# Kernel tuning notes

Measured on AMD Instinct MI355X. Metric: run time of the kernel, lower is better.

Reference implementation:

```python
import jax, jax.numpy as jnp
import numpy as np

N_ELEC, N_NUC, D, F, E = 1024, 256, 64, 64, 131072
HH, HG = 128, 128
# labels: en (elec->nuc), ne (nuc->elec), same (elec->elec), anti (elec->elec)
SRC_N = [N_ELEC, N_NUC, N_ELEC, N_ELEC]
TGT_N = [N_NUC, N_ELEC, N_ELEC, N_ELEC]


def setup_inputs() -> dict:
    key = jax.random.key(0)
    ks = jax.random.split(key, 16)
    s_elec = jax.random.normal(ks[0], (N_ELEC, D), jnp.float32)
    v_elec = jax.random.normal(ks[1], (N_ELEC, D, 3), jnp.float32)
    s_nuc = jax.random.normal(ks[2], (N_NUC, D), jnp.float32)
    v_nuc = jax.random.normal(ks[3], (N_NUC, D, 3), jnp.float32)
    senders = jnp.stack([jax.random.randint(jax.random.fold_in(ks[4], i), (E,), 0, SRC_N[i]) for i in range(4)]).astype(jnp.int32)
    receivers = jnp.stack([jax.random.randint(jax.random.fold_in(ks[5], i), (E,), 0, TGT_N[i]) for i in range(4)]).astype(jnp.int32)
    dist = jax.random.uniform(ks[6], (4, E, F), jnp.float32)
    dirs = jax.random.normal(ks[7], (4, E, 3), jnp.float32)
    dirs = dirs / jnp.linalg.norm(dirs, axis=-1, keepdims=True)  # unit directions
    def w_init(k, shape):
        return jax.random.normal(k, shape, jnp.float32) / jnp.sqrt(jnp.float32(shape[-2]))
    return {
        's_elec': s_elec, 'v_elec': v_elec, 's_nuc': s_nuc, 'v_nuc': v_nuc,
        'dist': dist, 'dirs': dirs,
        'W_w': w_init(ks[8], (4, F, 3 * D)),
        'W_h1': w_init(ks[9], (4, D, HH)), 'W_h2': w_init(ks[10], (4, HH, 3 * D)),
        'W_g1': w_init(ks[11], (4, 2 * D, HG)), 'W_g2': w_init(ks[12], (4, HG, 3 * D)),
        'W_V': jnp.broadcast_to(jnp.eye(D, dtype=jnp.float32), (4, D, D)),
        'W_U': jnp.broadcast_to(jnp.eye(D, dtype=jnp.float32), (4, D, D)),
        'senders': senders, 'receivers': receivers,
    }


def _painn_layer(s_elec, v_elec, s_nuc, v_nuc, dist, dirs, W_w, W_h1, W_h2, W_g1, W_g2, W_V, W_U, senders, receivers):
    src_s = [s_elec, s_nuc, s_elec, s_elec]
    src_v = [v_elec, v_nuc, v_elec, v_elec]
    ds_e = jnp.zeros_like(s_elec); dv_e = jnp.zeros_like(v_elec)
    ds_n = jnp.zeros_like(s_nuc); dv_n = jnp.zeros_like(v_nuc)
    for i in range(4):
        n_tgt = TGT_N[i]
        # edge MLPs: w (1-layer, last linear) and h (2-layer silu, last linear), bias-free
        we = dist[i] @ W_w[i]                                   # [E, 3D]
        h_all = jax.nn.silu(src_s[i] @ W_h1[i]) @ W_h2[i]        # [n_src, 3D]
        hx = h_all[senders[i]]                                   # gather per edge
        phi_s, phi_vv, phi_vs = jnp.split(we * hx, 3, axis=-1)   # each [E, D]
        z_s = jax.ops.segment_sum(phi_s, receivers[i], n_tgt)    # [n_tgt, D]
        vv = phi_vv[..., None] * src_v[i][senders[i]]            # [E, D, 3]
        vs = phi_vs[..., None] * dirs[i][:, None, :]             # [E, D, 3]
        z_v = jax.ops.segment_sum(vv + vs, receivers[i], n_tgt)  # [n_tgt, D, 3]
        Vv = jnp.einsum('ndi,df->nfi', z_v, W_V[i])
        Uv = jnp.einsum('ndi,df->nfi', z_v, W_U[i])
        g_in = jnp.concatenate([z_s, (Vv ** 2).sum(axis=-1)], axis=-1)  # [n_tgt, 2D]
        gs = jax.nn.silu(g_in @ W_g1[i]) @ W_g2[i]               # [n_tgt, 3D]
        a_ss, a_vv, a_sv = jnp.split(gs, 3, axis=-1)
        upd_v = Uv * a_vv[..., None]
        upd_s = a_sv * jnp.einsum('nfi,nfi->nf', Uv, Vv) + a_ss
        if i == 0:  # 'en' -> nuclei
            ds_n = ds_n + upd_s; dv_n = dv_n + upd_v
        else:       # 'ne','same','anti' -> electrons
            ds_e = ds_e + upd_s; dv_e = dv_e + upd_v
    s_e = s_elec + ds_e
    v_e = v_elec + dv_e
    return jnp.concatenate([s_e, v_e.reshape(N_ELEC, -1)], axis=-1)


def reference(s_elec, v_elec, s_nuc, v_nuc, dist, dirs, W_w, W_h1, W_h2, W_g1, W_g2, W_V, W_U, senders, receivers):
    return _painn_layer(s_elec, v_elec, s_nuc, v_nuc, dist, dirs, W_w, W_h1, W_h2, W_g1, W_g2, W_V, W_U, senders, receivers)
```

## Files before the change

### kernel.cpp

```cpp
#include <hip/hip_runtime.h>
#include <stdint.h>

#define E_EDGES 131072
#define NELEC 1024
#define NNUC 256
#define MAXCHUNK 256
#define ECHUNK 128
#define NBLK 16
#define UNPB 4

typedef unsigned short ushort_t;
typedef __attribute__((ext_vector_type(8))) short short8;
typedef __attribute__((ext_vector_type(4))) short short4_t;
typedef __attribute__((ext_vector_type(4))) float float4_t;
typedef __attribute__((ext_vector_type(8))) float float8_t;
typedef __attribute__((ext_vector_type(4))) int int4_t;
typedef __attribute__((ext_vector_type(2))) unsigned int uint2_t;

__device__ inline float silu_f(float x){ return x / (1.0f + expf(-x)); }

__device__ inline short f2bf_rne(float x){
    union { float f; uint32_t u; } a; a.f = x;
    return (short)((a.u + 0x7fffu + ((a.u >> 16) & 1u)) >> 16);
}
__device__ inline float bf2f(short h){
    union { uint32_t u; float f; } a; a.u = ((uint32_t)(uint16_t)h) << 16;
    return a.f;
}
__device__ inline ushort_t bfu(float x){ return (ushort_t)f2bf_rne(x); }
__device__ inline float asf_lo(uint32_t u){ union { uint32_t u; float f; } a; a.u = u << 16; return a.f; }
__device__ inline float asf_hi(uint32_t u){ union { uint32_t u; float f; } a; a.u = u & 0xFFFF0000u; return a.f; }

__global__ __launch_bounds__(256) void prep_kernel(
    const float* __restrict__ s_elec, const float* __restrict__ v_elec,
    const float* __restrict__ s_nuc,  const float* __restrict__ v_nuc,
    const float* __restrict__ W_h1, const float* __restrict__ W_h2,
    const float* __restrict__ W_w,
    const int* __restrict__ receivers,
    ushort_t* __restrict__ tabA, ushort_t* __restrict__ tabB,
    short* __restrict__ fragH, short* __restrict__ fragL,
    int* __restrict__ bh, float* __restrict__ out)
{
    int b = blockIdx.x, tid = threadIdx.x;
    __shared__ float sls[8][64];
    __shared__ float hidls[128][8];
    __shared__ int hist[1024];

    if (b < 288){
        int t, node0;
        if (b < 32){ t = 0; node0 = b*8; }
        else if (b < 160){ t = 1; node0 = (b-32)*8; }
        else { t = 2; node0 = (b-160)*8; }
        int tp = t + 1;
        const float* src = (t == 0) ? s_nuc : s_elec;
        const float* vsrc = (t == 0) ? v_nuc : v_elec;
        long baseA = (t == 0) ? 0 : (t == 1 ? 32768 : 163840);
        long baseB = (t == 0) ? 0 : (t == 1 ? 65536 : 327680);
        for (int i = tid; i < 512; i += 256){ int n = i >> 6, f = i & 63; sls[n][f] = src[(node0+n)*64 + f]; }
        __syncthreads();
        {
            int j = tid & 127, nh = tid >> 7;
            const float* w1 = W_h1 + (long)tp*64*128;
            float a0=0,a1=0,a2=0,a3=0;
            #pragma unroll 8
            for (int f = 0; f < 64; f++){
                float w = w1[f*128 + j];
                a0 += sls[nh*4+0][f]*w; a1 += sls[nh*4+1][f]*w;
                a2 += sls[nh*4+2][f]*w; a3 += sls[nh*4+3][f]*w;
            }
            float4_t hv = { silu_f(a0), silu_f(a1), silu_f(a2), silu_f(a3) };
            *(float4_t*)&hidls[j][nh*4] = hv;
        }
        __syncthreads();
        if (tid < 192){
            const float* w2 = W_h2 + (long)tp*128*192;
            float acc[8] = {0,0,0,0,0,0,0,0};
            #pragma unroll 4
            for (int h = 0; h < 128; h++){
                float w = w2[h*192 + tid];
                float4_t ha = *(float4_t*)&hidls[h][0];
                float4_t hb = *(float4_t*)&hidls[h][4];
                acc[0]+=ha[0]*w; acc[1]+=ha[1]*w; acc[2]+=ha[2]*w; acc[3]+=ha[3]*w;
                acc[4]+=hb[0]*w; acc[5]+=hb[1]*w; acc[6]+=hb[2]*w; acc[7]+=hb[3]*w;
            }
            int p = tid >> 6, d2 = tid & 63;
            if (p == 0){
                #pragma unroll
                for (int n = 0; n < 8; n++)
                    tabA[baseA + (long)((node0+n)*64 + d2)*2 + 0] = bfu(acc[n]);
            } else if (p == 2){
                #pragma unroll
                for (int n = 0; n < 8; n++)
                    tabA[baseA + (long)((node0+n)*64 + d2)*2 + 1] = bfu(acc[n]);
            } else {
                #pragma unroll
                for (int n = 0; n < 8; n++){
                    const float* vp = vsrc + (long)(node0+n)*192 + d2*3;
                    long o = baseB + (long)((node0+n)*64 + d2)*4;
                    tabB[o+0] = bfu(acc[n]*vp[0]);
                    tabB[o+1] = bfu(acc[n]*vp[1]);
                    tabB[o+2] = bfu(acc[n]*vp[2]);
                }
            }
        }
    } else if (b < 291){
        int t = b - 288, tp = t + 1;
        const float* W = W_w + (long)tp*64*192;
        for (int idx = tid; idx < 12288; idx += 256){
            int j    = idx & 7;
            int lane = (idx >> 3) & 63;
            int ks   = (idx >> 9) & 1;
            int nt   = idx >> 10;
            int k = ks*32 + ((lane >> 4) & 3)*8 + j;
            int n = nt*16 + (lane & 15);
            float v = W[k*192 + n];
            short hi = f2bf_rne(v);
            short lo = f2bf_rne(v - bf2f(hi));
            fragH[t*12288 + idx] = hi;
            fragL[t*12288 + idx] = lo;
        }
    } else if (b < 547){
        int i = (b - 291)*256 + tid;
        int n = i >> 6, c4 = i & 63;
        float4_t v;
        if (c4 < 16) v = *(const float4_t*)(s_elec + n*64 + c4*4);
        else         v = *(const float4_t*)(v_elec + n*192 + (c4-16)*4);
        *(float4_t*)(out + n*256 + c4*4) = v;
    } else {
        int hb = b - 547, t = hb >> 4, blk = hb & 15;
        for (int i = tid; i < 1024; i += 256) hist[i] = 0;
        __syncthreads();
        long base = (long)(t+1)*E_EDGES + blk*8192;
        #pragma unroll 4
        for (int it = 0; it < 32; it++){
            int r = receivers[base + it*256 + tid];
            atomicAdd(&hist[r], 1);
        }
        __syncthreads();
        for (int bin = tid; bin < 1024; bin += 256)
            bh[(t*1024 + bin)*NBLK + blk] = hist[bin];
    }
}

__global__ __launch_bounds__(1024) void scan_kernel(int* __restrict__ bh,
                                                    int* __restrict__ offs,
                                                    int* __restrict__ counts){
    __shared__ int buf[1024];
    int t = blockIdx.x;
    int tid = threadIdx.x;
    int base = (t*1024 + tid)*NBLK;
    int vals[NBLK];
    const int4_t* p = (const int4_t*)(bh + base);
    int s = 0;
    #pragma unroll
    for (int j = 0; j < NBLK/4; j++){
        int4_t x = p[j];
        vals[j*4+0]=x[0]; vals[j*4+1]=x[1]; vals[j*4+2]=x[2]; vals[j*4+3]=x[3];
        s += x[0]+x[1]+x[2]+x[3];
    }
    buf[tid] = s;
    __syncthreads();
    int x = s;
    for (int off = 1; off < 1024; off <<= 1){
        int y = (tid >= off) ? buf[tid - off] : 0;
        __syncthreads();
        x += y; buf[tid] = x;
        __syncthreads();
    }
    int run = t*E_EDGES + (x - s);
    offs[t*1024 + tid] = run;
    counts[t*1024 + tid] = s;
    #pragma unroll
    for (int j = 0; j < NBLK; j++){
        bh[base + j] = run;
        run += vals[j];
    }
}

__global__ __launch_bounds__(256) void scatter_kernel(const int* __restrict__ receivers,
                                                      const int* __restrict__ senders,
                                                      const int* __restrict__ bh,
                                                      int* __restrict__ sorted){
    int hb = blockIdx.x, t = hb >> 4, blk = hb & 15;
    int tid = threadIdx.x;
    __shared__ int cur[1024];
    for (int bin = tid; bin < 1024; bin += 256) cur[bin] = bh[(t*1024 + bin)*NBLK + blk];
    __syncthreads();
    long base = (long)(t+1)*E_EDGES + blk*8192;
    #pragma unroll 2
    for (int it = 0; it < 32; it++){
        int e = blk*8192 + it*256 + tid;
        int r = receivers[base + it*256 + tid];
        int snd = senders[base + it*256 + tid];
        int pos = atomicAdd(&cur[r], 1);
        sorted[pos] = e | (snd << 17);
    }
}

__global__ __launch_bounds__(256) void edge_kernel(
    const float* __restrict__ dist, const float* __restrict__ dirs,
    const ushort_t* __restrict__ tabA, const ushort_t* __restrict__ tabB,
    const short* __restrict__ fragH, const short* __restrict__ fragL,
    const int* __restrict__ counts, const int* __restrict__ offs, const int* __restrict__ sorted,
    float* __restrict__ zbuf)
{
    int b = blockIdx.x;
    int t = b >> 10, node = b & 1023;
    const ushort_t* ta = tabA + ((t == 0) ? 0 : (t == 1 ? 32768 : 163840));
    const ushort_t* tb = tabB + ((t == 0) ? 0 : (t == 1 ? 65536 : 327680));
    const float* dbase = dist + (long)(t+1)*E_EDGES*64;
    const float* dirbase = dirs + (long)(t+1)*E_EDGES*3;

    int tid = threadIdx.x;
    int w = tid >> 6, l = tid & 63;
    int q = l >> 4, c16 = l & 15;
    int d = w*16 + c16;
    int se = tid >> 1, sk = tid & 1;

    __shared__ short AHs[ECHUNK*64];
    __shared__ short ALs[ECHUNK*64];
    __shared__ int sid[ECHUNK];
    __shared__ float dls[ECHUNK][3];

    short8 bhf[3][2], blf[3][2];
    #pragma unroll
    for (int ni = 0; ni < 3; ni++){
        int nt = w + ni*4;
        #pragma unroll
        for (int ks = 0; ks < 2; ks++){
            long base = (long)t*12288 + ((nt*2 + ks)*64 + l)*8;
            bhf[ni][ks] = *(const short8*)(fragH + base);
            blf[ni][ks] = *(const short8*)(fragL + base);
        }
    }

    float acc_s = 0.f, acc_v0 = 0.f, acc_v1 = 0.f, acc_v2 = 0.f;

    int deg   = counts[t*1024 + node];
    int start = offs[t*1024 + node];

    const float4_t z4 = {0.f,0.f,0.f,0.f};
    const float8_t z8 = {0.f,0.f,0.f,0.f,0.f,0.f,0.f,0.f};

    for (int cbase = 0; cbase < deg; cbase += ECHUNK){
        int chunk = deg - cbase; if (chunk > ECHUNK) chunk = ECHUNK;
        __syncthreads();

        bool okA = (se < chunk);
        int vA = okA ? sorted[(long)start + cbase + se] : 0;
        if (tid < ECHUNK){
            int v = (tid < chunk) ? sorted[(long)start + cbase + tid] : 0;
            sid[tid] = ((unsigned)v) >> 17;
            float d0=0.f, d1=0.f, d2=0.f;
            if (tid < chunk){
                const float* dp = dirbase + (long)(v & 131071)*3;
                d0 = dp[0]; d1 = dp[1]; d2 = dp[2];
            }
            dls[tid][0]=d0; dls[tid][1]=d1; dls[tid][2]=d2;
        }
        {
            long ebase = okA ? ((long)(vA & 131071)*64 + sk*32) : 0;
            #pragma unroll
            for (int j = 0; j < 4; j++){
                float8_t f = z8;
                if (okA) f = *(const float8_t*)(dbase + ebase + j*8);
                short8 h8, l8;
                #pragma unroll
                for (int jj = 0; jj < 8; jj++){
                    short hi = f2bf_rne(f[jj]);
                    h8[jj] = hi;
                    l8[jj] = f2bf_rne(f[jj] - bf2f(hi));
                }
                int slot = (sk*4 + j) ^ (se & 7);
                *(short8*)&AHs[se*64 + slot*8] = h8;
                *(short8*)&ALs[se*64 + slot*8] = l8;
            }
        }
        __syncthreads();

        int ngroups = (chunk + 15) >> 4;
        for (int g = 0; g < ngroups; g++){
            int mrb = g*16 + q*4;
            uint32_t gA[4]; uint2_t gB[4];
            #pragma unroll
            for (int r = 0; r < 4; r++){
                int s = sid[mrb + r];
                gA[r] = *(const uint32_t*)(ta + (long)(s*64 + d)*2);
                gB[r] = *(const uint2_t*)(tb + (long)(s*64 + d)*4);
            }
            int e  = g*16 + c16;
            int sw = e & 7;
            int o0 = e*64 + ((q ^ sw) * 8);
            int o1 = e*64 + (((4 + q) ^ sw) * 8);
            short8 ah0 = *(short8*)&AHs[o0];
            short8 ah1 = *(short8*)&AHs[o1];
            short8 al0 = *(short8*)&ALs[o0];
            short8 al1 = *(short8*)&ALs[o1];

            float4_t C[3];
            #pragma unroll
            for (int ni = 0; ni < 3; ni++){
                float4_t acc = z4;
                acc = __builtin_amdgcn_mfma_f32_16x16x32_bf16(ah0, bhf[ni][0], acc, 0, 0, 0);
                acc = __builtin_amdgcn_mfma_f32_16x16x32_bf16(ah1, bhf[ni][1], acc, 0, 0, 0);
                acc = __builtin_amdgcn_mfma_f32_16x16x32_bf16(ah0, blf[ni][0], acc, 0, 0, 0);
                acc = __builtin_amdgcn_mfma_f32_16x16x32_bf16(ah1, blf[ni][1], acc, 0, 0, 0);
                acc = __builtin_amdgcn_mfma_f32_16x16x32_bf16(al0, bhf[ni][0], acc, 0, 0, 0);
                acc = __builtin_amdgcn_mfma_f32_16x16x32_bf16(al1, bhf[ni][1], acc, 0, 0, 0);
                C[ni] = acc;
            }

            #pragma unroll
            for (int r = 0; r < 4; r++){
                int mr = mrb + r;
                float hs  = asf_lo(gA[r]);
                float hvs = asf_hi(gA[r]);
                float hv0 = asf_lo(gB[r][0]);
                float hv1 = asf_hi(gB[r][0]);
                float hv2 = asf_lo(gB[r][1]);
                acc_s += C[0][r] * hs;
                float pvs = C[2][r] * hvs;
                acc_v0 += C[1][r]*hv0 + pvs * dls[mr][0];
                acc_v1 += C[1][r]*hv1 + pvs * dls[mr][1];
                acc_v2 += C[1][r]*hv2 + pvs * dls[mr][2];
            }
        }
    }

    acc_s  += __shfl_xor(acc_s, 16);  acc_s  += __shfl_xor(acc_s, 32);
    acc_v0 += __shfl_xor(acc_v0, 16); acc_v0 += __shfl_xor(acc_v0, 32);
    acc_v1 += __shfl_xor(acc_v1, 16); acc_v1 += __shfl_xor(acc_v1, 32);
    acc_v2 += __shfl_xor(acc_v2, 16); acc_v2 += __shfl_xor(acc_v2, 32);
    if (l < 16){
        float* zp = zbuf + ((long)(t*1024 + node))*256;
        zp[d] = acc_s;
        zp[64 + d*3 + 0] = acc_v0;
        zp[64 + d*3 + 1] = acc_v1;
        zp[64 + d*3 + 2] = acc_v2;
    }
}

__global__ __launch_bounds__(256) void update_kernel(
    const float* __restrict__ W_V, const float* __restrict__ W_U,
    const float* __restrict__ W_g1, const float* __restrict__ W_g2,
    const float* __restrict__ zbuf, float* __restrict__ out)
{
    int b = blockIdx.x;
    int t = b >> 8, tp = t + 1;
    int nb = (b & 255) * UNPB;
    int tid = threadIdx.x;

    __shared__ float zls[UNPB][256];
    __shared__ float Vv[UNPB][64][3], Uv[UNPB][64][3];
    __shared__ float gin[UNPB][128];
    __shared__ float hid[UNPB][128];
    __shared__ float aL[UNPB][192];
    __shared__ float vdot[UNPB][64];

    {
        int n = tid >> 6, c = tid & 63;
        *(float4_t*)&zls[n][c*4] =
            *(const float4_t*)(zbuf + ((long)(t*1024 + nb + n))*256 + c*4);
    }
    __syncthreads();

    {
        int f = tid & 63, n = tid >> 6;
        const float* wv = W_V + (long)tp*4096;
        const float* wu = W_U + (long)tp*4096;
        float av0=0,av1=0,av2=0,au0=0,au1=0,au2=0;
        #pragma unroll 4
        for (int dd = 0; dd < 64; dd++){
            float wvv = wv[dd*64 + f], wuu = wu[dd*64 + f];
            float z0 = zls[n][64 + dd*3 + 0];
            float z1 = zls[n][64 + dd*3 + 1];
            float z2 = zls[n][64 + dd*3 + 2];
            av0 += z0*wvv; av1 += z1*wvv; av2 += z2*wvv;
            au0 += z0*wuu; au1 += z1*wuu; au2 += z2*wuu;
        }
        Vv[n][f][0]=av0; Vv[n][f][1]=av1; Vv[n][f][2]=av2;
        Uv[n][f][0]=au0; Uv[n][f][1]=au1; Uv[n][f][2]=au2;
    }
    __syncthreads();

    {
        int n = tid >> 6, f = tid & 63;
        float v0=Vv[n][f][0], v1=Vv[n][f][1], v2=Vv[n][f][2];
        float u0=Uv[n][f][0], u1=Uv[n][f][1], u2=Uv[n][f][2];
        gin[n][f]      = zls[n][f];
        gin[n][64 + f] = v0*v0 + v1*v1 + v2*v2;
        vdot[n][f]     = u0*v0 + u1*v1 + u2*v2;
    }
    __syncthreads();

    {
        int h = tid & 127, ng = tid >> 7;
        const float* w1 = W_g1 + (long)tp*16384;
        float a0=0, a1=0;
        #pragma unroll 4
        for (int c = 0; c < 128; c++){
            float w = w1[c*128 + h];
            a0 += gin[ng*2+0][c]*w;
            a1 += gin[ng*2+1][c]*w;
        }
        hid[ng*2+0][h] = silu_f(a0);
        hid[ng*2+1][h] = silu_f(a1);
    }
    __syncthreads();

    if (tid < 192){
        const float* w2 = W_g2 + (long)tp*24576;
        float a0=0,a1=0,a2=0,a3=0;
        #pragma unroll 4
        for (int h = 0; h < 128; h++){
            float w = w2[h*192 + tid];
            a0 += hid[0][h]*w; a1 += hid[1][h]*w;
            a2 += hid[2][h]*w; a3 += hid[3][h]*w;
        }
        aL[0][tid]=a0; aL[1][tid]=a1; aL[2][tid]=a2; aL[3][tid]=a3;
    }
    __syncthreads();

    {
        int n = tid >> 6, f = tid & 63;
        float upd = aL[n][128 + f]*vdot[n][f] + aL[n][f];
        atomicAdd(&out[(nb + n)*256 + f], upd);
        float g = aL[n][64 + f];
        #pragma unroll
        for (int i = 0; i < 3; i++){
            float updv = Uv[n][f][i] * g;
            atomicAdd(&out[(nb + n)*256 + 64 + f*3 + i], updv);
        }
    }
}

__global__ __launch_bounds__(256) void main_kernel(
    const float* __restrict__ dist, const float* __restrict__ dirs,
    const float* __restrict__ W_V, const float* __restrict__ W_U,
    const float* __restrict__ W_g1, const float* __restrict__ W_g2,
    const ushort_t* __restrict__ tabA, const ushort_t* __restrict__ tabB,
    const short* __restrict__ fragH, const short* __restrict__ fragL,
    const int* __restrict__ counts, const int* __restrict__ offs, const int* __restrict__ sorted,
    float* __restrict__ out)
{
    int b = blockIdx.x;
    int t = b >> 10, node = b & 1023, tp = t + 1;
    const ushort_t* ta = tabA + ((t == 0) ? 0 : (t == 1 ? 32768 : 163840));
    const ushort_t* tb = tabB + ((t == 0) ? 0 : (t == 1 ? 65536 : 327680));
    const float* dbase = dist + (long)tp*E_EDGES*64;
    const float* dirbase = dirs + (long)tp*E_EDGES*3;

    int tid = threadIdx.x;
    int w = tid >> 6, l = tid & 63;
    int q = l >> 4, c16 = l & 15;
    int d = w*16 + c16;

    __shared__ short AH[2][2][64][8];
    __shared__ short AL[2][2][64][8];
    __shared__ float dls[2][16][3];
    __shared__ int eid[MAXCHUNK];
    __shared__ int sid[MAXCHUNK];
    __shared__ float zs[64];
    __shared__ float zv[64][3];
    __shared__ float VvL[192], UvL[192];
    __shared__ float gin[128], hidl[128], aLrr[192], vdotL[64];

    short8 bhf[3][2], blf[3][2];
    #pragma unroll
    for (int ni = 0; ni < 3; ni++){
        int nt = w + ni*4;
        #pragma unroll
        for (int ks = 0; ks < 2; ks++){
            long base = (long)t*12288 + ((nt*2 + ks)*64 + l)*8;
            bhf[ni][ks] = *(const short8*)(fragH + base);
            blf[ni][ks] = *(const short8*)(fragL + base);
        }
    }

    float acc_s = 0.f, acc_v0 = 0.f, acc_v1 = 0.f, acc_v2 = 0.f;

    int deg   = counts[t*1024 + node];
    int start = offs[t*1024 + node];

    int m = tid >> 4, seg = tid & 15;
    int ks_w = seg >> 3, quad_w = (seg >> 1) & 3, j0_w = (seg & 1)*4;
    int lane2 = m | (quad_w << 4);
    int mm = tid / 3, ii = tid - mm*3;

    const float4_t z4 = {0.f,0.f,0.f,0.f};

    for (int cbase = 0; cbase < deg; cbase += MAXCHUNK){
        int chunk = deg - cbase; if (chunk > MAXCHUNK) chunk = MAXCHUNK;
        __syncthreads();
        {
            int v = 0;
            if (tid < chunk) v = sorted[(long)start + cbase + tid];
            eid[tid] = v & 131071;
            sid[tid] = ((unsigned)v) >> 17;
        }
        __syncthreads();

        int ngroups = (chunk + 15) >> 4;
        float4_t dv = z4;
        if (m < chunk) dv = *(const float4_t*)(dbase + (long)eid[m]*64 + seg*4);
        float dirv = 0.f;
        if (tid < 48 && mm < chunk) dirv = dirbase[(long)eid[mm]*3 + ii];
        uint32_t gA[4]; uint2_t gB[4];
        #pragma unroll
        for (int r = 0; r < 4; r++){
            int s = sid[q*4 + r];
            gA[r] = *(const uint32_t*)(ta + (long)(s*64 + d)*2);
            gB[r] = *(const uint2_t*)(tb + (long)(s*64 + d)*4);
        }

        for (int g = 0; g < ngroups; g++){
            int buf = g & 1;
            {
                short4_t h4, l4;
                #pragma unroll
                for (int jj = 0; jj < 4; jj++){
                    short hi = f2bf_rne(dv[jj]);
                    h4[jj] = hi;
                    l4[jj] = f2bf_rne(dv[jj] - bf2f(hi));
                }
                *(short4_t*)&AH[buf][ks_w][lane2][j0_w] = h4;
                *(short4_t*)&AL[buf][ks_w][lane2][j0_w] = l4;
                if (tid < 48) dls[buf][mm][ii] = dirv;
            }
            float4_t dvn = z4; float dirn = 0.f;
            uint32_t gAn[4] = {0,0,0,0}; uint2_t gBn[4] = {{0,0},{0,0},{0,0},{0,0}};
            if (g + 1 < ngroups){
                int li = (g+1)*16 + m;
                if (li < chunk) dvn = *(const float4_t*)(dbase + (long)eid[li]*64 + seg*4);
                int li2 = (g+1)*16 + mm;
                if (tid < 48 && li2 < chunk) dirn = dirbase[(long)eid[li2]*3 + ii];
                #pragma unroll
                for (int r = 0; r < 4; r++){
                    int s = sid[(g+1)*16 + q*4 + r];
                    gAn[r] = *(const uint32_t*)(ta + (long)(s*64 + d)*2);
                    gBn[r] = *(const uint2_t*)(tb + (long)(s*64 + d)*4);
                }
            }
            __syncthreads();

            short8 ah0 = *(short8*)&AH[buf][0][l][0];
            short8 ah1 = *(short8*)&AH[buf][1][l][0];
            short8 al0 = *(short8*)&AL[buf][0][l][0];
            short8 al1 = *(short8*)&AL[buf][1][l][0];
            float4_t C[3];
            #pragma unroll
            for (int ni = 0; ni < 3; ni++){
                float4_t acc = z4;
                acc = __builtin_amdgcn_mfma_f32_16x16x32_bf16(ah0, bhf[ni][0], acc, 0, 0, 0);
                acc = __builtin_amdgcn_mfma_f32_16x16x32_bf16(ah1, bhf[ni][1], acc, 0, 0, 0);
                acc = __builtin_amdgcn_mfma_f32_16x16x32_bf16(ah0, blf[ni][0], acc, 0, 0, 0);
                acc = __builtin_amdgcn_mfma_f32_16x16x32_bf16(ah1, blf[ni][1], acc, 0, 0, 0);
                acc = __builtin_amdgcn_mfma_f32_16x16x32_bf16(al0, bhf[ni][0], acc, 0, 0, 0);
                acc = __builtin_amdgcn_mfma_f32_16x16x32_bf16(al1, bhf[ni][1], acc, 0, 0, 0);
                C[ni] = acc;
            }

            #pragma unroll
            for (int r = 0; r < 4; r++){
                int mr = q*4 + r;
                float hs  = asf_lo(gA[r]);
                float hvs = asf_hi(gA[r]);
                float hv0 = asf_lo(gB[r][0]);
                float hv1 = asf_hi(gB[r][0]);
                float hv2 = asf_lo(gB[r][1]);
                acc_s += C[0][r] * hs;
                float pvs = C[2][r] * hvs;
                acc_v0 += C[1][r]*hv0 + pvs * dls[buf][mr][0];
                acc_v1 += C[1][r]*hv1 + pvs * dls[buf][mr][1];
                acc_v2 += C[1][r]*hv2 + pvs * dls[buf][mr][2];
            }
            dv = dvn; dirv = dirn;
            #pragma unroll
            for (int r = 0; r < 4; r++){ gA[r] = gAn[r]; gB[r] = gBn[r]; }
        }
    }

    acc_s  += __shfl_xor(acc_s, 16);  acc_s  += __shfl_xor(acc_s, 32);
    acc_v0 += __shfl_xor(acc_v0, 16); acc_v0 += __shfl_xor(acc_v0, 32);
    acc_v1 += __shfl_xor(acc_v1, 16); acc_v1 += __shfl_xor(acc_v1, 32);
    acc_v2 += __shfl_xor(acc_v2, 16); acc_v2 += __shfl_xor(acc_v2, 32);
    __syncthreads();
    if (l < 16){
        zs[d] = acc_s;
        zv[d][0] = acc_v0; zv[d][1] = acc_v1; zv[d][2] = acc_v2;
    }
    __syncthreads();

    if (tid < 192){
        int i = tid >> 6, f = tid & 63;
        const float* wv = W_V + (long)tp*64*64;
        const float* wu = W_U + (long)tp*64*64;
        float av = 0.f, au = 0.f;
        #pragma unroll 8
        for (int dd = 0; dd < 64; dd++){
            float z = zv[dd][i];
            av += z * wv[dd*64 + f];
            au += z * wu[dd*64 + f];
        }
        VvL[f*3 + i] = av;
        UvL[f*3 + i] = au;
    }
    __syncthreads();
    if (tid < 64){
        int f = tid;
        float v0 = VvL[f*3], v1 = VvL[f*3+1], v2 = VvL[f*3+2];
        float u0 = UvL[f*3], u1 = UvL[f*3+1], u2 = UvL[f*3+2];
        gin[f] = zs[f];
        gin[64 + f] = v0*v0 + v1*v1 + v2*v2;
        vdotL[f] = u0*v0 + u1*v1 + u2*v2;
    }
    __syncthreads();
    if (tid < 128){
        const float* w1 = W_g1 + (long)tp*128*128;
        float acc = 0.f;
        #pragma unroll 8
        for (int c = 0; c < 128; c++) acc += gin[c] * w1[c*128 + tid];
        hidl[tid] = silu_f(acc);
    }
    __syncthreads();
    if (tid < 192){
        const float* w2 = W_g2 + (long)tp*128*192;
        float acc = 0.f;
        #pragma unroll 8
        for (int h = 0; h < 128; h++) acc += hidl[h] * w2[h*192 + tid];
        aLrr[tid] = acc;
    }
    __syncthreads();
    if (tid < 64){
        int f = tid;
        float upd = aLrr[128 + f] * vdotL[f] + aLrr[f];
        atomicAdd(&out[node*256 + f], upd);
    }
    if (tid < 192){
        int i = tid >> 6, f = tid & 63;
        float updv = UvL[f*3 + i] * aLrr[64 + f];
        atomicAdd(&out[node*256 + 64 + f*3 + i], updv);
    }
}

extern "C" void kernel_launch(void* const* d_in, const int* in_sizes, int n_in,
                              void* d_out, int out_size, void* d_ws, size_t ws_size,
                              hipStream_t stream){
    const float* s_elec  = (const float*)d_in[0];
    const float* v_elec  = (const float*)d_in[1];
    const float* s_nuc   = (const float*)d_in[2];
    const float* v_nuc   = (const float*)d_in[3];
    const float* dist    = (const float*)d_in[4];
    const float* dirs    = (const float*)d_in[5];
    const float* W_w     = (const float*)d_in[6];
    const float* W_h1    = (const float*)d_in[7];
    const float* W_h2    = (const float*)d_in[8];
    const float* W_g1    = (const float*)d_in[9];
    const float* W_g2    = (const float*)d_in[10];
    const float* W_V     = (const float*)d_in[11];
    const float* W_U     = (const float*)d_in[12];
    const int* senders   = (const int*)d_in[13];
    const int* receivers = (const int*)d_in[14];
    float* out = (float*)d_out;
    char* ws = (char*)d_ws;

    ushort_t* tabA  = (ushort_t*)(ws + 0);
    ushort_t* tabB  = (ushort_t*)(ws + 589824);
    short* fragH  = (short*)(ws + 1769472);
    short* fragL  = (short*)(ws + 1843200);
    int*   bh     = (int*)  (ws + 1916928);
    int*   offs   = (int*)  (ws + 2113536);
    int*   counts = (int*)  (ws + 2125824);
    int*   sorted = (int*)  (ws + 2138112);
    float* zbuf   = (float*)(ws + 3710976);
    if (ws_size < 3710976) return;
    bool split = (ws_size >= 6856704);

    prep_kernel<<<dim3(595), dim3(256), 0, stream>>>(
        s_elec, v_elec, s_nuc, v_nuc, W_h1, W_h2, W_w, receivers,
        tabA, tabB, fragH, fragL, bh, out);
    scan_kernel<<<dim3(3), dim3(1024), 0, stream>>>(bh, offs, counts);
    scatter_kernel<<<dim3(48), dim3(256), 0, stream>>>(receivers, senders, bh, sorted);
    if (split){
        edge_kernel<<<dim3(3072), dim3(256), 0, stream>>>(
            dist, dirs, tabA, tabB, fragH, fragL, counts, offs, sorted, zbuf);
        update_kernel<<<dim3(768), dim3(256), 0, stream>>>(
            W_V, W_U, W_g1, W_g2, zbuf, out);
    } else {
        main_kernel<<<dim3(3072), dim3(256), 0, stream>>>(
            dist, dirs, W_V, W_U, W_g1, W_g2,
            tabA, tabB, fragH, fragL, counts, offs, sorted, out);
    }
}
```

Measured before the change: 344.9 us.

## Load edge features directly into MFMA registers, dropping LDS staging and barriers

The edge kernel no longer stages 128-edge chunks of distance features, sender ids and directions in shared memory behind two block barriers. Each wave now loads its 16 edges' features straight from global memory into the MFMA operand layout, and shares sender ids and directions through wave shuffles. The fp32-to-bf16 hi/lo split now uses the packed v_cvt_pk_bf16_f32 instruction instead of manual rounding. This removes LDS use and block synchronisation and may raise occupancy. In exchange, all four waves read the same edge rows, so global and cache traffic for the distance features grows up to fourfold.

```diff
diff --git a/kernel.cpp b/kernel.cpp
--- a/kernel.cpp
+++ b/kernel.cpp
@@ -5,7 +5,6 @@
 #define NELEC 1024
 #define NNUC 256
 #define MAXCHUNK 256
-#define ECHUNK 128
 #define NBLK 16
 #define UNPB 4
 
@@ -215,12 +214,6 @@
     int w = tid >> 6, l = tid & 63;
     int q = l >> 4, c16 = l & 15;
     int d = w*16 + c16;
-    int se = tid >> 1, sk = tid & 1;
-
-    __shared__ short AHs[ECHUNK*64];
-    __shared__ short ALs[ECHUNK*64];
-    __shared__ int sid[ECHUNK];
-    __shared__ float dls[ECHUNK][3];
 
     short8 bhf[3][2], blf[3][2];
     #pragma unroll
@@ -240,90 +233,77 @@
     int start = offs[t*1024 + node];
 
     const float4_t z4 = {0.f,0.f,0.f,0.f};
-    const float8_t z8 = {0.f,0.f,0.f,0.f,0.f,0.f,0.f,0.f};
-
-    for (int cbase = 0; cbase < deg; cbase += ECHUNK){
-        int chunk = deg - cbase; if (chunk > ECHUNK) chunk = ECHUNK;
-        __syncthreads();
-
-        bool okA = (se < chunk);
-        int vA = okA ? sorted[(long)start + cbase + se] : 0;
-        if (tid < ECHUNK){
-            int v = (tid < chunk) ? sorted[(long)start + cbase + tid] : 0;
-            sid[tid] = ((unsigned)v) >> 17;
-            float d0=0.f, d1=0.f, d2=0.f;
-            if (tid < chunk){
-                const float* dp = dirbase + (long)(v & 131071)*3;
-                d0 = dp[0]; d1 = dp[1]; d2 = dp[2];
-            }
-            dls[tid][0]=d0; dls[tid][1]=d1; dls[tid][2]=d2;
-        }
-        {
-            long ebase = okA ? ((long)(vA & 131071)*64 + sk*32) : 0;
-            #pragma unroll
-            for (int j = 0; j < 4; j++){
-                float8_t f = z8;
-                if (okA) f = *(const float8_t*)(dbase + ebase + j*8);
-                short8 h8, l8;
-                #pragma unroll
-                for (int jj = 0; jj < 8; jj++){
-                    short hi = f2bf_rne(f[jj]);
-                    h8[jj] = hi;
-                    l8[jj] = f2bf_rne(f[jj] - bf2f(hi));
-                }
-                int slot = (sk*4 + j) ^ (se & 7);
-                *(short8*)&AHs[se*64 + slot*8] = h8;
-                *(short8*)&ALs[se*64 + slot*8] = l8;
-            }
-        }
-        __syncthreads();
-
-        int ngroups = (chunk + 15) >> 4;
-        for (int g = 0; g < ngroups; g++){
-            int mrb = g*16 + q*4;
-            uint32_t gA[4]; uint2_t gB[4];
-            #pragma unroll
-            for (int r = 0; r < 4; r++){
-                int s = sid[mrb + r];
-                gA[r] = *(const uint32_t*)(ta + (long)(s*64 + d)*2);
-                gB[r] = *(const uint2_t*)(tb + (long)(s*64 + d)*4);
-            }
-            int e  = g*16 + c16;
-            int sw = e & 7;
-            int o0 = e*64 + ((q ^ sw) * 8);
-            int o1 = e*64 + (((4 + q) ^ sw) * 8);
-            short8 ah0 = *(short8*)&AHs[o0];
-            short8 ah1 = *(short8*)&AHs[o1];
-            short8 al0 = *(short8*)&ALs[o0];
-            short8 al1 = *(short8*)&ALs[o1];
-
-            float4_t C[3];
-            #pragma unroll
-            for (int ni = 0; ni < 3; ni++){
-                float4_t acc = z4;
-                acc = __builtin_amdgcn_mfma_f32_16x16x32_bf16(ah0, bhf[ni][0], acc, 0, 0, 0);
-                acc = __builtin_amdgcn_mfma_f32_16x16x32_bf16(ah1, bhf[ni][1], acc, 0, 0, 0);
-                acc = __builtin_amdgcn_mfma_f32_16x16x32_bf16(ah0, blf[ni][0], acc, 0, 0, 0);
-                acc = __builtin_amdgcn_mfma_f32_16x16x32_bf16(ah1, blf[ni][1], acc, 0, 0, 0);
-                acc = __builtin_amdgcn_mfma_f32_16x16x32_bf16(al0, bhf[ni][0], acc, 0, 0, 0);
-                acc = __builtin_amdgcn_mfma_f32_16x16x32_bf16(al1, bhf[ni][1], acc, 0, 0, 0);
-                C[ni] = acc;
-            }
-
-            #pragma unroll
-            for (int r = 0; r < 4; r++){
-                int mr = mrb + r;
-                float hs  = asf_lo(gA[r]);
-                float hvs = asf_hi(gA[r]);
-                float hv0 = asf_lo(gB[r][0]);
-                float hv1 = asf_hi(gB[r][0]);
-                float hv2 = asf_lo(gB[r][1]);
-                acc_s += C[0][r] * hs;
-                float pvs = C[2][r] * hvs;
-                acc_v0 += C[1][r]*hv0 + pvs * dls[mr][0];
-                acc_v1 += C[1][r]*hv1 + pvs * dls[mr][1];
-                acc_v2 += C[1][r]*hv2 + pvs * dls[mr][2];
-            }
+
+    for (int e0 = 0; e0 < deg; e0 += 16){
+        int rem = deg - e0;
+        int ridx = (c16 < rem) ? c16 : 0;
+        int sA = sorted[(long)start + e0 + ridx];
+        long eA = (long)(sA & 131071);
+        const float* dp = dbase + eA*64 + q*8;
+        float8_t f0 = *(const float8_t*)(dp);
+        float8_t f1 = *(const float8_t*)(dp + 32);
+        float dir0 = dirbase[eA*3 + 0];
+        float dir1 = dirbase[eA*3 + 1];
+        float dir2 = dirbase[eA*3 + 2];
+
+        union { int4_t i; short8 s; } H0, L0, H1, L1;
+        #pragma unroll
+        for (int j = 0; j < 4; j++){
+            float a0 = f0[2*j], a1 = f0[2*j+1];
+            uint32_t hp, lp;
+            asm("v_cvt_pk_bf16_f32 %0, %1, %2" : "=v"(hp) : "v"(a0), "v"(a1));
+            float r0 = asf_lo(hp), r1 = asf_hi(hp);
+            asm("v_cvt_pk_bf16_f32 %0, %1, %2" : "=v"(lp) : "v"(a0 - r0), "v"(a1 - r1));
+            H0.i[j] = (int)hp; L0.i[j] = (int)lp;
+            float b0 = f1[2*j], b1 = f1[2*j+1];
+            uint32_t hq, lq;
+            asm("v_cvt_pk_bf16_f32 %0, %1, %2" : "=v"(hq) : "v"(b0), "v"(b1));
+            float s0 = asf_lo(hq), s1 = asf_hi(hq);
+            asm("v_cvt_pk_bf16_f32 %0, %1, %2" : "=v"(lq) : "v"(b0 - s0), "v"(b1 - s1));
+            H1.i[j] = (int)hq; L1.i[j] = (int)lq;
+        }
+        short8 ah0 = H0.s, al0 = L0.s, ah1 = H1.s, al1 = L1.s;
+
+        uint32_t gA[4]; uint2_t gB[4];
+        float dls0[4], dls1[4], dls2[4];
+        #pragma unroll
+        for (int r = 0; r < 4; r++){
+            int srcl = q*4 + r;
+            int sr = __shfl(sA, srcl);
+            int s = ((unsigned)sr) >> 17;
+            gA[r] = *(const uint32_t*)(ta + (long)(s*64 + d)*2);
+            gB[r] = *(const uint2_t*)(tb + (long)(s*64 + d)*4);
+            dls0[r] = __shfl(dir0, srcl);
+            dls1[r] = __shfl(dir1, srcl);
+            dls2[r] = __shfl(dir2, srcl);
+        }
+
+        float4_t C[3];
+        #pragma unroll
+        for (int ni = 0; ni < 3; ni++){
+            float4_t acc = z4;
+            acc = __builtin_amdgcn_mfma_f32_16x16x32_bf16(ah0, bhf[ni][0], acc, 0, 0, 0);
+            acc = __builtin_amdgcn_mfma_f32_16x16x32_bf16(ah1, bhf[ni][1], acc, 0, 0, 0);
+            acc = __builtin_amdgcn_mfma_f32_16x16x32_bf16(ah0, blf[ni][0], acc, 0, 0, 0);
+            acc = __builtin_amdgcn_mfma_f32_16x16x32_bf16(ah1, blf[ni][1], acc, 0, 0, 0);
+            acc = __builtin_amdgcn_mfma_f32_16x16x32_bf16(al0, bhf[ni][0], acc, 0, 0, 0);
+            acc = __builtin_amdgcn_mfma_f32_16x16x32_bf16(al1, bhf[ni][1], acc, 0, 0, 0);
+            C[ni] = acc;
+        }
+
+        #pragma unroll
+        for (int r = 0; r < 4; r++){
+            bool ok = (q*4 + r) < rem;
+            float hs  = ok ? asf_lo(gA[r]) : 0.f;
+            float hvs = ok ? asf_hi(gA[r]) : 0.f;
+            float hv0 = ok ? asf_lo(gB[r][0]) : 0.f;
+            float hv1 = ok ? asf_hi(gB[r][0]) : 0.f;
+            float hv2 = ok ? asf_lo(gB[r][1]) : 0.f;
+            acc_s += C[0][r] * hs;
+            float pvs = C[2][r] * hvs;
+            acc_v0 += C[1][r]*hv0 + pvs * dls0[r];
+            acc_v1 += C[1][r]*hv1 + pvs * dls1[r];
+            acc_v2 += C[1][r]*hv2 + pvs * dls2[r];
         }
     }
 
```

After: 396.2 us. 14.9% more time.
